# Kernel tuning notes

Measured on AMD Instinct MI355X. Metric: run time of the kernel, lower is better.

Reference implementation:

```python
import jax, jax.numpy as jnp
import numpy as np

B, T, CODE_NUM, MED_NUM = 256, 32, 4880, 1000
CODE_SIZE, H, OUT = 128, 128, 4880


def setup_inputs() -> dict:
    key = jax.random.key(0)
    ks = jax.random.split(key, 16)
    code_x = (jax.random.uniform(ks[0], (B, T, CODE_NUM)) < 0.05).astype(jnp.float32)
    medicine_codes = (jax.random.uniform(ks[1], (B, T, MED_NUM)) < 0.02).astype(jnp.float32)
    divided = (jax.random.uniform(ks[2], (B, T, CODE_NUM)) < 0.05).astype(jnp.float32)
    neighbors = (jax.random.uniform(ks[3], (B, T, CODE_NUM)) < 0.05).astype(jnp.float32)
    lens = jax.random.randint(ks[4], (B,), 1, T + 1)
    s = lambda fan: 1.0 / np.sqrt(fan)
    c_emb = jax.random.normal(ks[5], (CODE_NUM, CODE_SIZE)) * s(CODE_SIZE)
    m_emb = jax.random.normal(ks[6], (MED_NUM, CODE_SIZE)) * s(CODE_SIZE)
    W_c = jax.random.normal(ks[7], (CODE_SIZE, H)) * s(CODE_SIZE)
    W_m = jax.random.normal(ks[8], (CODE_SIZE, H)) * s(CODE_SIZE)
    Wa = jax.random.normal(ks[9], (3 * H, 32)) * s(3 * H)
    ba = jnp.zeros((32,), jnp.float32)
    va = jax.random.normal(ks[10], (32,)) * s(32)
    W_cls = jax.random.normal(ks[11], (3 * H, OUT)) * s(3 * H)
    b_cls = jnp.zeros((OUT,), jnp.float32)
    return dict(code_x=code_x, divided=divided, neighbors=neighbors, lens=lens,
                medicine_codes=medicine_codes, c_emb=c_emb, m_emb=m_emb,
                W_c=W_c, W_m=W_m, Wa=Wa, ba=ba, va=va, W_cls=W_cls, b_cls=b_cls)


def _forward(code_x, medicine_codes, lens, c_emb, m_emb, W_c, W_m, Wa, ba, va, W_cls, b_cls):
    # hypergraph_part: transform code/med embeddings, aggregate active codes per visit
    Hc = jnp.tanh(c_emb @ W_c)                      # [code_num, H]
    Hm = jnp.tanh(m_emb @ W_m)                      # [med_num, H]
    sum_c = jnp.einsum('btc,ch->bth', code_x, Hc)   # masked sum over active dx codes
    sum_m = jnp.einsum('btm,mh->bth', medicine_codes, Hm)
    h_c = sum_c / jnp.clip(code_x.sum(-1, keepdims=True), 1.0, None)
    h_m = sum_m / jnp.clip(medicine_codes.sum(-1, keepdims=True), 1.0, None)
    repre = jnp.concatenate([h_c, h_m, h_c * h_m], axis=-1)  # [B,T,3H]
    # DotProductAttention over visits, masked by lens
    scores = jnp.einsum('btk,k->bt', jnp.tanh(repre @ Wa + ba), va)
    mask = jnp.arange(T)[None, :] < lens[:, None]
    attn = jax.nn.softmax(jnp.where(mask, scores, -1e9), axis=-1)
    ctx = jnp.einsum('bt,btd->bd', attn, repre)     # [B,3H]
    # Classifier (dropout=identity in eval) + sigmoid
    return jax.nn.sigmoid(ctx @ W_cls + b_cls)      # [B,OUT]


def reference(code_x, divided, neighbors, lens, medicine_codes, c_emb, m_emb,
              W_c, W_m, Wa, ba, va, W_cls, b_cls):
    # divided/neighbors feed the transition branch whose output is unused
    # in the original forward's final prediction path.
    return _forward(code_x, medicine_codes, lens, c_emb, m_emb,
                    W_c, W_m, Wa, ba, va, W_cls, b_cls)
```

## Files before the change

### kernel.cpp

```cpp
#include <hip/hip_runtime.h>
#include <hip/hip_bf16.h>
#include <math.h>

#define Bsz 256
#define Tn 32
#define CODEN 4880
#define MEDN 1000
#define Hdim 128
#define OUTN 4880
#define R3H 384
#define RSTR 256
#define KC_PAD 4928
#define KM_PAD 1024
#define NSC 77
#define NSM 16

typedef unsigned short u16;
typedef __attribute__((ext_vector_type(4))) float f32x4;
typedef __attribute__((ext_vector_type(8))) short s16x8;
typedef __attribute__((ext_vector_type(4))) unsigned int u32x4;

union PKU { u32x4 u; s16x8 s; };

__device__ inline unsigned f2bf(float f) {
  unsigned u = __float_as_uint(f);
  return (u + 0x7fffu + ((u >> 16) & 1u)) >> 16;
}
__device__ inline unsigned pack2(float f0, float f1) {
  return (__float_as_uint(f0) >> 16) | (__float_as_uint(f1) & 0xffff0000u);
}

__global__ __launch_bounds__(128) void k_emb(
    const float* __restrict__ c_emb, const float* __restrict__ m_emb,
    const float* __restrict__ W_c, const float* __restrict__ W_m,
    u16* __restrict__ HcT, u16* __restrict__ HmT) {
  int blk = blockIdx.x, h = threadIdx.x;
  bool is_med = blk >= KC_PAD;
  int c = is_med ? blk - KC_PAD : blk;
  int n = is_med ? MEDN : CODEN;
  u16* dst = is_med ? (HmT + (size_t)h * KM_PAD + c) : (HcT + (size_t)h * KC_PAD + c);
  if (c >= n) { *dst = 0; return; }
  const float* emb = (is_med ? m_emb : c_emb) + (size_t)c * Hdim;
  const float* W = is_med ? W_m : W_c;
  __shared__ float e[Hdim];
  e[h] = emb[h];
  __syncthreads();
  float acc = 0.f;
#pragma unroll 8
  for (int k = 0; k < Hdim; ++k) acc += e[k] * W[k * Hdim + h];
  *dst = (u16)f2bf(tanhf(acc));
}

__device__ inline void stageB(const u16* __restrict__ Bt, int k0, int ldk,
                              u16* __restrict__ buf, int tid) {
#pragma unroll
  for (int it = 0; it < 4; ++it) {
    int c = it * 256 + tid;
    const u16* src = Bt + (size_t)(c & 127) * ldk + k0 + (c >> 7) * 8;
#if __has_builtin(__builtin_amdgcn_global_load_lds)
    __builtin_amdgcn_global_load_lds(
        (const __attribute__((address_space(1))) void*)src,
        (__attribute__((address_space(3))) void*)(buf + c * 8), 16, 0, 0);
#else
    *(u32x4*)(buf + c * 8) = *(const u32x4*)src;
#endif
  }
}

__device__ inline void loadA(const float* __restrict__ Arow, int k0, int kmax,
                             float4* A) {
  int kb = k0;
  A[0] = (kb +  4 <= kmax) ? *(const float4*)(Arow + kb)      : make_float4(0,0,0,0);
  A[1] = (kb +  8 <= kmax) ? *(const float4*)(Arow + kb + 4)  : make_float4(0,0,0,0);
  A[2] = (kb + 36 <= kmax) ? *(const float4*)(Arow + kb + 32) : make_float4(0,0,0,0);
  A[3] = (kb + 40 <= kmax) ? *(const float4*)(Arow + kb + 36) : make_float4(0,0,0,0);
}

__global__ __launch_bounds__(256, 4) void k_gemm(
    const float* __restrict__ code_x, const float* __restrict__ med,
    const u16* __restrict__ HcT, const u16* __restrict__ HmT,
    float* __restrict__ repre) {
  __shared__ u16 Bb[2][8192];
  int gid = blockIdx.x;
  bool is_med = gid >= 512;
  int sg = is_med ? gid - 512 : gid;
  int b = sg >> 1, half = sg & 1;
  int tid = threadIdx.x;
  int w = tid >> 6, l = tid & 63;
  int l15 = l & 15, sub = l >> 4;
  int row_g = b * Tn + half * 16 + l15;

  const float* Arow; const u16* Bt; int NS, kmax, ldk, cbase;
  if (is_med) { Arow = med    + (size_t)row_g * MEDN;  Bt = HmT; NS = NSM; kmax = MEDN;  ldk = KM_PAD; cbase = 128; }
  else        { Arow = code_x + (size_t)row_g * CODEN; Bt = HcT; NS = NSC; kmax = CODEN; ldk = KC_PAD; cbase = 0; }

  f32x4 acc[2] = {{0.f,0.f,0.f,0.f},{0.f,0.f,0.f,0.f}};
  float cnt = 0.f;
  float4 A[4], nA[4];

  stageB(Bt, 0, ldk, Bb[0], tid);
  loadA(Arow, sub * 8, kmax, A);

  for (int s = 0; s < NS; ++s) {
    __syncthreads();
    int cur = s & 1;
    if (s + 1 < NS) {
      stageB(Bt, (s + 1) * 64, ldk, Bb[cur ^ 1], tid);
      loadA(Arow, (s + 1) * 64 + sub * 8, kmax, nA);
    }
    PKU pa0, pa1;
    pa0.u[0] = pack2(A[0].x, A[0].y); pa0.u[1] = pack2(A[0].z, A[0].w);
    pa0.u[2] = pack2(A[1].x, A[1].y); pa0.u[3] = pack2(A[1].z, A[1].w);
    pa1.u[0] = pack2(A[2].x, A[2].y); pa1.u[1] = pack2(A[2].z, A[2].w);
    pa1.u[2] = pack2(A[3].x, A[3].y); pa1.u[3] = pack2(A[3].z, A[3].w);
#pragma unroll
    for (int q = 0; q < 4; ++q)
      cnt += A[q].x + A[q].y + A[q].z + A[q].w;
    const u16* bbuf = Bb[cur];
#pragma unroll
    for (int f = 0; f < 2; ++f) {
      int col = (w * 2 + f) * 16 + l15;
      PKU pb0, pb1;
      pb0.u = *(const u32x4*)(bbuf + ((size_t)(0 * 4 + sub) * 128 + col) * 8);
      pb1.u = *(const u32x4*)(bbuf + ((size_t)(1 * 4 + sub) * 128 + col) * 8);
      acc[f] = __builtin_amdgcn_mfma_f32_16x16x32_bf16(pa0.s, pb0.s, acc[f], 0, 0, 0);
      acc[f] = __builtin_amdgcn_mfma_f32_16x16x32_bf16(pa1.s, pb1.s, acc[f], 0, 0, 0);
    }
#pragma unroll
    for (int q = 0; q < 4; ++q) A[q] = nA[q];
  }

  cnt += __shfl_xor(cnt, 16, 64);
  cnt += __shfl_xor(cnt, 32, 64);

#pragma unroll
  for (int j = 0; j < 4; ++j) {
    int r = sub * 4 + j;
    float cr = __shfl(cnt, r, 64);
    float iv = 1.0f / fmaxf(cr, 1.0f);
    size_t rbase = (size_t)(b * Tn + half * 16 + r) * RSTR + cbase;
#pragma unroll
    for (int f = 0; f < 2; ++f)
      repre[rbase + (w * 2 + f) * 16 + l15] = acc[f][j] * iv;
  }
}

__global__ __launch_bounds__(256) void k_post(
    const float* __restrict__ repre, const float* __restrict__ Wa,
    const float* __restrict__ ba, const float* __restrict__ va,
    const int* __restrict__ lens, float* __restrict__ ctx) {
  __shared__ float rep_s[Tn][R3H + 4];
  __shared__ float sc_s[Tn];
  __shared__ float at_s[Tn];
  int b = blockIdx.x, tid = threadIdx.x;

  for (int i = tid; i < Tn * (RSTR / 4); i += 256) {
    int t = i >> 6, c4 = i & 63;
    f32x4 v = *(const f32x4*)(repre + (size_t)(b * Tn + t) * RSTR + c4 * 4);
    *(f32x4*)&rep_s[t][c4 * 4] = v;
  }
  __syncthreads();
  for (int i = tid; i < Tn * 128; i += 256) {
    int t = i >> 7, c = i & 127;
    rep_s[t][256 + c] = rep_s[t][c] * rep_s[t][128 + c];
  }
  __syncthreads();
  {
    int t = tid >> 3, j0 = (tid & 7) * 4;
    float u0 = 0.f, u1 = 0.f, u2 = 0.f, u3 = 0.f;
    for (int k = 0; k < R3H; ++k) {
      float r = rep_s[t][k];
      float4 wv = *(const float4*)(Wa + k * 32 + j0);
      u0 += r * wv.x; u1 += r * wv.y; u2 += r * wv.z; u3 += r * wv.w;
    }
    float sv = tanhf(u0 + ba[j0])     * va[j0]
             + tanhf(u1 + ba[j0 + 1]) * va[j0 + 1]
             + tanhf(u2 + ba[j0 + 2]) * va[j0 + 2]
             + tanhf(u3 + ba[j0 + 3]) * va[j0 + 3];
    sv += __shfl_xor(sv, 1, 64);
    sv += __shfl_xor(sv, 2, 64);
    sv += __shfl_xor(sv, 4, 64);
    if ((tid & 7) == 0) sc_s[t] = sv;
  }
  __syncthreads();
  if (tid < Tn) {
    int len = lens[b];
    float s = sc_s[tid];
    bool valid = tid < len;
    float sm = valid ? s : -1e30f;
    float m = sm;
#pragma unroll
    for (int off = 16; off >= 1; off >>= 1) m = fmaxf(m, __shfl_xor(m, off, 32));
    float e = valid ? expf(sm - m) : 0.f;
    float su = e;
#pragma unroll
    for (int off = 16; off >= 1; off >>= 1) su += __shfl_xor(su, off, 32);
    at_s[tid] = e / su;
  }
  __syncthreads();
  for (int d = tid; d < R3H; d += 256) {
    float a = 0.f;
#pragma unroll
    for (int t = 0; t < Tn; ++t) a += at_s[t] * rep_s[t][d];
    ctx[(size_t)b * R3H + d] = a;
  }
}

__device__ inline void fma4(float4& a, float s, const float4& w) {
  a.x += s * w.x; a.y += s * w.y; a.z += s * w.z; a.w += s * w.w;
}

__global__ __launch_bounds__(256) void k_cls(
    const float* __restrict__ ctx, const float* __restrict__ W_cls,
    const float* __restrict__ b_cls, float* __restrict__ out) {
  __shared__ float cs_t[R3H * 8];
  int tid = threadIdx.x;
  int ob = blockIdx.x % 5;
  int b0 = (blockIdx.x / 5) * 8;
  for (int i = tid; i < R3H * 8; i += 256) {
    int k = i >> 3, r = i & 7;
    cs_t[i] = ctx[(size_t)(b0 + r) * R3H + k];
  }
  __syncthreads();
  int o0 = ob * 1024 + tid * 4;
  if (o0 >= OUTN) return;
  float4 acc[8];
#pragma unroll
  for (int r = 0; r < 8; ++r) acc[r] = make_float4(0.f, 0.f, 0.f, 0.f);
  const float* wp = W_cls + o0;
  for (int k = 0; k < R3H; k += 8) {
    float4 wv[8];
#pragma unroll
    for (int u = 0; u < 8; ++u) wv[u] = *(const float4*)(wp + (size_t)(k + u) * OUTN);
#pragma unroll
    for (int u = 0; u < 8; ++u) {
      float4 cA = *(const float4*)&cs_t[(k + u) * 8];
      float4 cB = *(const float4*)&cs_t[(k + u) * 8 + 4];
      fma4(acc[0], cA.x, wv[u]); fma4(acc[1], cA.y, wv[u]);
      fma4(acc[2], cA.z, wv[u]); fma4(acc[3], cA.w, wv[u]);
      fma4(acc[4], cB.x, wv[u]); fma4(acc[5], cB.y, wv[u]);
      fma4(acc[6], cB.z, wv[u]); fma4(acc[7], cB.w, wv[u]);
    }
  }
  float4 bc = *(const float4*)(b_cls + o0);
#pragma unroll
  for (int r = 0; r < 8; ++r) {
    float4 v;
    v.x = 1.f / (1.f + expf(-(acc[r].x + bc.x)));
    v.y = 1.f / (1.f + expf(-(acc[r].y + bc.y)));
    v.z = 1.f / (1.f + expf(-(acc[r].z + bc.z)));
    v.w = 1.f / (1.f + expf(-(acc[r].w + bc.w)));
    *(float4*)(out + (size_t)(b0 + r) * OUTN + o0) = v;
  }
}

extern "C" void kernel_launch(void* const* d_in, const int* in_sizes, int n_in,
                              void* d_out, int out_size, void* d_ws, size_t ws_size,
                              hipStream_t stream) {
  const float* code_x = (const float*)d_in[0];
  const int*   lens   = (const int*)d_in[3];
  const float* med    = (const float*)d_in[4];
  const float* c_emb  = (const float*)d_in[5];
  const float* m_emb  = (const float*)d_in[6];
  const float* W_c    = (const float*)d_in[7];
  const float* W_m    = (const float*)d_in[8];
  const float* Wa     = (const float*)d_in[9];
  const float* ba     = (const float*)d_in[10];
  const float* va     = (const float*)d_in[11];
  const float* W_cls  = (const float*)d_in[12];
  const float* b_cls  = (const float*)d_in[13];
  float* out = (float*)d_out;

  u16* HcT = (u16*)d_ws;
  u16* HmT = HcT + (size_t)128 * KC_PAD;
  float* repre = (float*)(HmT + (size_t)128 * KM_PAD);
  float* ctx = repre + (size_t)Bsz * Tn * RSTR;

  hipLaunchKernelGGL(k_emb, dim3(KC_PAD + KM_PAD), dim3(128), 0, stream,
                     c_emb, m_emb, W_c, W_m, HcT, HmT);
  hipLaunchKernelGGL(k_gemm, dim3(1024), dim3(256), 0, stream,
                     code_x, med, HcT, HmT, repre);
  hipLaunchKernelGGL(k_post, dim3(Bsz), dim3(256), 0, stream,
                     repre, Wa, ba, va, lens, ctx);
  hipLaunchKernelGGL(k_cls, dim3(160), dim3(256), 0, stream,
                     ctx, W_cls, b_cls, out);
}
```

Before: 609.6 us.

## Restructure visit-aggregation GEMM into single-wave split-K tiles with register-loaded B

The aggregation GEMM now runs one 64-thread wave per 16-row stripe. Each wave covers all 128 output columns with eight MFMA accumulators and loads B fragments straight from global memory into registers, replacing the shared-memory staging and block barriers. The code-matrix reduction is split in two along K, with partial sums and row counts written to workspace and combined and normalized in the post kernel. This removes LDS traffic and synchronization and adds parallelism. The cost is reloading B per wave, with less reuse across rows, plus extra partial-sum writes and reads.

```diff
diff --git a/kernel.cpp b/kernel.cpp
--- a/kernel.cpp
+++ b/kernel.cpp
@@ -9,11 +9,13 @@
 #define Hdim 128
 #define OUTN 4880
 #define R3H 384
-#define RSTR 256
-#define KC_PAD 4928
+#define KC_PAD 4992
 #define KM_PAD 1024
-#define NSC 77
-#define NSM 16
+#define NSPLIT 2
+#define KSPL (KC_PAD / NSPLIT)
+#define NSC (KSPL / 32)
+#define NSM (KM_PAD / 32)
+#define NROW (Bsz * Tn)
 
 typedef unsigned short u16;
 typedef __attribute__((ext_vector_type(4))) float f32x4;
@@ -51,113 +53,118 @@
   *dst = (u16)f2bf(tanhf(acc));
 }
 
-__device__ inline void stageB(const u16* __restrict__ Bt, int k0, int ldk,
-                              u16* __restrict__ buf, int tid) {
-#pragma unroll
-  for (int it = 0; it < 4; ++it) {
-    int c = it * 256 + tid;
-    const u16* src = Bt + (size_t)(c & 127) * ldk + k0 + (c >> 7) * 8;
-#if __has_builtin(__builtin_amdgcn_global_load_lds)
-    __builtin_amdgcn_global_load_lds(
-        (const __attribute__((address_space(1))) void*)src,
-        (__attribute__((address_space(3))) void*)(buf + c * 8), 16, 0, 0);
-#else
-    *(u32x4*)(buf + c * 8) = *(const u32x4*)src;
-#endif
-  }
-}
-
-__device__ inline void loadA(const float* __restrict__ Arow, int k0, int kmax,
-                             float4* A) {
-  int kb = k0;
-  A[0] = (kb +  4 <= kmax) ? *(const float4*)(Arow + kb)      : make_float4(0,0,0,0);
-  A[1] = (kb +  8 <= kmax) ? *(const float4*)(Arow + kb + 4)  : make_float4(0,0,0,0);
-  A[2] = (kb + 36 <= kmax) ? *(const float4*)(Arow + kb + 32) : make_float4(0,0,0,0);
-  A[3] = (kb + 40 <= kmax) ? *(const float4*)(Arow + kb + 36) : make_float4(0,0,0,0);
-}
-
-__global__ __launch_bounds__(256, 4) void k_gemm(
+__device__ inline void loadA2(const float* __restrict__ Arow, int kb, int kmax,
+                              float4& a0, float4& a1) {
+  a0 = (kb + 4 <= kmax) ? *(const float4*)(Arow + kb)     : make_float4(0.f,0.f,0.f,0.f);
+  a1 = (kb + 8 <= kmax) ? *(const float4*)(Arow + kb + 4) : make_float4(0.f,0.f,0.f,0.f);
+}
+
+#define GSTEP(CA0, CA1, CB, NA0, NA1, NB, K0, PF)                              \
+  {                                                                            \
+    if (PF) {                                                                  \
+      loadA2(Arow, (K0) + 32 + sub * 8, kmax, NA0, NA1);                       \
+      _Pragma("unroll")                                                        \
+      for (int f = 0; f < 8; ++f) NB[f] = *(const u32x4*)(Bp[f] + (K0) + 32);  \
+    }                                                                          \
+    cnt += CA0.x + CA0.y + CA0.z + CA0.w + CA1.x + CA1.y + CA1.z + CA1.w;      \
+    PKU pa;                                                                    \
+    pa.u[0] = pack2(CA0.x, CA0.y); pa.u[1] = pack2(CA0.z, CA0.w);              \
+    pa.u[2] = pack2(CA1.x, CA1.y); pa.u[3] = pack2(CA1.z, CA1.w);              \
+    _Pragma("unroll")                                                          \
+    for (int f = 0; f < 8; ++f) {                                              \
+      PKU pb; pb.u = CB[f];                                                    \
+      acc[f] = __builtin_amdgcn_mfma_f32_16x16x32_bf16(pa.s, pb.s, acc[f], 0, 0, 0); \
+    }                                                                          \
+  }
+
+__global__ __launch_bounds__(64, 3) void k_gemm(
     const float* __restrict__ code_x, const float* __restrict__ med,
     const u16* __restrict__ HcT, const u16* __restrict__ HmT,
-    float* __restrict__ repre) {
-  __shared__ u16 Bb[2][8192];
-  int gid = blockIdx.x;
-  bool is_med = gid >= 512;
-  int sg = is_med ? gid - 512 : gid;
-  int b = sg >> 1, half = sg & 1;
-  int tid = threadIdx.x;
-  int w = tid >> 6, l = tid & 63;
+    float* __restrict__ pc, float* __restrict__ pm,
+    float* __restrict__ cntc, float* __restrict__ cntm) {
+  int gw = blockIdx.x;
+  int l = threadIdx.x;
   int l15 = l & 15, sub = l >> 4;
-  int row_g = b * Tn + half * 16 + l15;
-
-  const float* Arow; const u16* Bt; int NS, kmax, ldk, cbase;
-  if (is_med) { Arow = med    + (size_t)row_g * MEDN;  Bt = HmT; NS = NSM; kmax = MEDN;  ldk = KM_PAD; cbase = 128; }
-  else        { Arow = code_x + (size_t)row_g * CODEN; Bt = HcT; NS = NSC; kmax = CODEN; ldk = KC_PAD; cbase = 0; }
-
-  f32x4 acc[2] = {{0.f,0.f,0.f,0.f},{0.f,0.f,0.f,0.f}};
+
+  bool is_med = gw >= 1024;
+  int stripe, NS, kbase, kmax, ldk;
+  const float* Aptr; const u16* Bt; float* pout; float* cout;
+  if (!is_med) {
+    int split = gw & 1; stripe = gw >> 1;
+    NS = NSC; kbase = split * KSPL; kmax = CODEN; ldk = KC_PAD;
+    Aptr = code_x; Bt = HcT;
+    pout = pc + (size_t)split * NROW * 128;
+    cout = cntc + split * NROW;
+  } else {
+    stripe = gw - 1024;
+    NS = NSM; kbase = 0; kmax = MEDN; ldk = KM_PAD;
+    Aptr = med; Bt = HmT;
+    pout = pm; cout = cntm;
+  }
+  int row_g = stripe * 16 + l15;
+  const float* Arow = Aptr + (size_t)row_g * kmax;
+  const u16* Bp[8];
+#pragma unroll
+  for (int f = 0; f < 8; ++f)
+    Bp[f] = Bt + (size_t)(f * 16 + l15) * ldk + sub * 8;
+
+  f32x4 acc[8];
+#pragma unroll
+  for (int f = 0; f < 8; ++f) acc[f] = (f32x4){0.f, 0.f, 0.f, 0.f};
   float cnt = 0.f;
-  float4 A[4], nA[4];
-
-  stageB(Bt, 0, ldk, Bb[0], tid);
-  loadA(Arow, sub * 8, kmax, A);
-
-  for (int s = 0; s < NS; ++s) {
-    __syncthreads();
-    int cur = s & 1;
-    if (s + 1 < NS) {
-      stageB(Bt, (s + 1) * 64, ldk, Bb[cur ^ 1], tid);
-      loadA(Arow, (s + 1) * 64 + sub * 8, kmax, nA);
-    }
-    PKU pa0, pa1;
-    pa0.u[0] = pack2(A[0].x, A[0].y); pa0.u[1] = pack2(A[0].z, A[0].w);
-    pa0.u[2] = pack2(A[1].x, A[1].y); pa0.u[3] = pack2(A[1].z, A[1].w);
-    pa1.u[0] = pack2(A[2].x, A[2].y); pa1.u[1] = pack2(A[2].z, A[2].w);
-    pa1.u[2] = pack2(A[3].x, A[3].y); pa1.u[3] = pack2(A[3].z, A[3].w);
-#pragma unroll
-    for (int q = 0; q < 4; ++q)
-      cnt += A[q].x + A[q].y + A[q].z + A[q].w;
-    const u16* bbuf = Bb[cur];
-#pragma unroll
-    for (int f = 0; f < 2; ++f) {
-      int col = (w * 2 + f) * 16 + l15;
-      PKU pb0, pb1;
-      pb0.u = *(const u32x4*)(bbuf + ((size_t)(0 * 4 + sub) * 128 + col) * 8);
-      pb1.u = *(const u32x4*)(bbuf + ((size_t)(1 * 4 + sub) * 128 + col) * 8);
-      acc[f] = __builtin_amdgcn_mfma_f32_16x16x32_bf16(pa0.s, pb0.s, acc[f], 0, 0, 0);
-      acc[f] = __builtin_amdgcn_mfma_f32_16x16x32_bf16(pa1.s, pb1.s, acc[f], 0, 0, 0);
-    }
-#pragma unroll
-    for (int q = 0; q < 4; ++q) A[q] = nA[q];
+  float4 A0, A1, N0, N1;
+  u32x4 Bv[8], Nv[8];
+
+  loadA2(Arow, kbase + sub * 8, kmax, A0, A1);
+#pragma unroll
+  for (int f = 0; f < 8; ++f) Bv[f] = *(const u32x4*)(Bp[f] + kbase);
+
+  for (int s = 0; s < NS; s += 2) {
+    int k0 = kbase + s * 32;
+    GSTEP(A0, A1, Bv, N0, N1, Nv, k0, true);
+    GSTEP(N0, N1, Nv, A0, A1, Bv, k0 + 32, s + 2 < NS);
   }
 
   cnt += __shfl_xor(cnt, 16, 64);
   cnt += __shfl_xor(cnt, 32, 64);
+  if (l < 16) cout[row_g] = cnt;
 
 #pragma unroll
   for (int j = 0; j < 4; ++j) {
     int r = sub * 4 + j;
-    float cr = __shfl(cnt, r, 64);
-    float iv = 1.0f / fmaxf(cr, 1.0f);
-    size_t rbase = (size_t)(b * Tn + half * 16 + r) * RSTR + cbase;
-#pragma unroll
-    for (int f = 0; f < 2; ++f)
-      repre[rbase + (w * 2 + f) * 16 + l15] = acc[f][j] * iv;
+    size_t rb = (size_t)(stripe * 16 + r) * 128;
+#pragma unroll
+    for (int f = 0; f < 8; ++f)
+      pout[rb + f * 16 + l15] = acc[f][j];
   }
 }
 
 __global__ __launch_bounds__(256) void k_post(
-    const float* __restrict__ repre, const float* __restrict__ Wa,
-    const float* __restrict__ ba, const float* __restrict__ va,
-    const int* __restrict__ lens, float* __restrict__ ctx) {
+    const float* __restrict__ pc, const float* __restrict__ pm,
+    const float* __restrict__ cntc, const float* __restrict__ cntm,
+    const float* __restrict__ Wa, const float* __restrict__ ba,
+    const float* __restrict__ va, const int* __restrict__ lens,
+    float* __restrict__ ctx) {
   __shared__ float rep_s[Tn][R3H + 4];
   __shared__ float sc_s[Tn];
   __shared__ float at_s[Tn];
   int b = blockIdx.x, tid = threadIdx.x;
 
-  for (int i = tid; i < Tn * (RSTR / 4); i += 256) {
-    int t = i >> 6, c4 = i & 63;
-    f32x4 v = *(const f32x4*)(repre + (size_t)(b * Tn + t) * RSTR + c4 * 4);
-    *(f32x4*)&rep_s[t][c4 * 4] = v;
+  for (int i = tid; i < Tn * 32; i += 256) {
+    int t = i >> 5, c4 = (i & 31) * 4;
+    size_t rb = (size_t)(b * Tn + t) * 128 + c4;
+    f32x4 s = {0.f, 0.f, 0.f, 0.f};
+#pragma unroll
+    for (int sp = 0; sp < NSPLIT; ++sp)
+      s += *(const f32x4*)(pc + (size_t)sp * NROW * 128 + rb);
+    float cn = 0.f;
+#pragma unroll
+    for (int sp = 0; sp < NSPLIT; ++sp) cn += cntc[sp * NROW + b * Tn + t];
+    s *= 1.f / fmaxf(cn, 1.f);
+    *(f32x4*)&rep_s[t][c4] = s;
+    f32x4 m = *(const f32x4*)(pm + rb);
+    m *= 1.f / fmaxf(cntm[b * Tn + t], 1.f);
+    *(f32x4*)&rep_s[t][128 + c4] = m;
   }
   __syncthreads();
   for (int i = tid; i < Tn * 128; i += 256) {
@@ -273,15 +280,18 @@
 
   u16* HcT = (u16*)d_ws;
   u16* HmT = HcT + (size_t)128 * KC_PAD;
-  float* repre = (float*)(HmT + (size_t)128 * KM_PAD);
-  float* ctx = repre + (size_t)Bsz * Tn * RSTR;
+  float* pc   = (float*)(HmT + (size_t)128 * KM_PAD);
+  float* pm   = pc + (size_t)NSPLIT * NROW * 128;
+  float* cntc = pm + (size_t)NROW * 128;
+  float* cntm = cntc + NSPLIT * NROW;
+  float* ctx  = cntm + NROW;
 
   hipLaunchKernelGGL(k_emb, dim3(KC_PAD + KM_PAD), dim3(128), 0, stream,
                      c_emb, m_emb, W_c, W_m, HcT, HmT);
-  hipLaunchKernelGGL(k_gemm, dim3(1024), dim3(256), 0, stream,
-                     code_x, med, HcT, HmT, repre);
+  hipLaunchKernelGGL(k_gemm, dim3(1024 + 512), dim3(64), 0, stream,
+                     code_x, med, HcT, HmT, pc, pm, cntc, cntm);
   hipLaunchKernelGGL(k_post, dim3(Bsz), dim3(256), 0, stream,
-                     repre, Wa, ba, va, lens, ctx);
+                     pc, pm, cntc, cntm, Wa, ba, va, lens, ctx);
   hipLaunchKernelGGL(k_cls, dim3(160), dim3(256), 0, stream,
                      ctx, W_cls, b_cls, out);
 }
```

New measurement: 607.6 us. No clear change (-0.3%).
